# Optimization experiments

Hardware: AMD Instinct MI355X
Metric: run time of the kernel (lower is better)

## Reference

```python
import jax, jax.numpy as jnp
import numpy as np

N = 50000      # nodes
E = 800000     # edges
IN = 128       # in_channels
HID = 128      # hidden_channels
OUT = 2        # out_channels (edge classes)
HEADS = 8      # EGConv default num_heads
BASES = 4      # EGConv default num_bases
FH = HID // HEADS  # per-head feature dim = 16


def _egconv(x, Wb, Wc, bc, b, row, col, norm, n):
    """One EGConv layer (aggregators=['symnorm']), self-loops already in row/col/norm.
    Wb: [in, BASES*FH] basis projection (no bias).
    Wc: [in, HEADS*BASES], bc: combination weights linear.
    b : [HID] output bias.
    """
    bases = x @ Wb                                            # [n, BASES*FH]
    msg = bases[row] * norm[:, None]                          # gather + symnorm scale
    agg = jax.ops.segment_sum(msg, col, num_segments=n)       # scatter-add -> [n, BASES*FH]
    w = (x @ Wc + bc).reshape(n, HEADS, BASES)                # per-node combination weights
    out = jnp.einsum('nhb,nbf->nhf', w, agg.reshape(n, BASES, FH))
    return out.reshape(n, HEADS * FH) + b


def setup_inputs() -> dict:
    key = jax.random.key(0)
    ks = jax.random.split(key, 12)
    s = 0.05
    inp = {
        'x': jax.random.normal(ks[0], (N, IN), jnp.float32),
        'edge_index': jax.random.randint(ks[1], (2, E), 0, N, jnp.int64),
        # conv1
        'Wb1': jax.random.normal(ks[2], (IN, BASES * FH), jnp.float32) * s,
        'Wc1': jax.random.normal(ks[3], (IN, HEADS * BASES), jnp.float32) * s,
        'bc1': jnp.zeros((HEADS * BASES,), jnp.float32),
        'b1': jnp.zeros((HID,), jnp.float32),
        # conv2
        'Wb2': jax.random.normal(ks[4], (HID, BASES * FH), jnp.float32) * s,
        'Wc2': jax.random.normal(ks[5], (HID, HEADS * BASES), jnp.float32) * s,
        'bc2': jnp.zeros((HEADS * BASES,), jnp.float32),
        'b2': jnp.zeros((HID,), jnp.float32),
        # edge classifier
        'Wcls': jax.random.normal(ks[6], (2 * HID, OUT), jnp.float32) * s,
        'bcls': jnp.zeros((OUT,), jnp.float32),
    }
    return inp


def reference(x, edge_index, Wb1, Wc1, bc1, b1, Wb2, Wc2, bc2, b2, Wcls, bcls):
    n = x.shape[0]
    # add self loops (EGConv default add_self_loops=True) + gcn_norm symnorm weights
    sl = jnp.arange(n, dtype=edge_index.dtype)
    row = jnp.concatenate([edge_index[0], sl])
    col = jnp.concatenate([edge_index[1], sl])
    deg = jax.ops.segment_sum(jnp.ones(row.shape[0], x.dtype), col, num_segments=n)
    dis = jnp.where(deg > 0, deg, 1.0) ** -0.5
    dis = jnp.where(deg > 0, dis, 0.0)
    norm = dis[row] * dis[col]                                # symnorm edge weight

    h = jax.nn.relu(_egconv(x, Wb1, Wc1, bc1, b1, row, col, norm, n))
    h = _egconv(h, Wb2, Wc2, bc2, b2, row, col, norm, n)

    # edge classifier: gather endpoint embeddings of ORIGINAL edges, concat, linear
    e = jnp.concatenate([h[edge_index[0]], h[edge_index[1]]], axis=-1)  # [E, 2*HID]
    return e @ Wcls + bcls
```

## Files before the change

### kernel.cpp

```cpp
#include <hip/hip_runtime.h>
#include <hip/hip_fp16.h>

#define NN 50000
#define EE 800000
#define NB_E2 1563

__global__ void k_count(const int* __restrict__ ei, int* cnt) {
    int t = blockIdx.x * 256 + threadIdx.x;
    if (t < EE / 2) {
        int2 cc = *(const int2*)(ei + EE + 2 * t);
        atomicAdd(&cnt[cc.x], 1);
        atomicAdd(&cnt[cc.y], 1);
    }
}

__global__ void k_scan1(const int* __restrict__ cnt, int* sloc, int* bsum,
                        float* dis, int n) {
    __shared__ int s[256];
    int tid = threadIdx.x;
    int i = blockIdx.x * 256 + tid;
    int v = (i < n) ? cnt[i] : 0;
    if (i < n) dis[i] = rsqrtf((float)v + 1.0f);
    s[tid] = v;
    __syncthreads();
    for (int off = 1; off < 256; off <<= 1) {
        int t2 = 0;
        if (tid >= off) t2 = s[tid - off];
        __syncthreads();
        if (tid >= off) s[tid] += t2;
        __syncthreads();
    }
    if (i < n) sloc[i] = s[tid] - v;
    if (tid == 255) bsum[blockIdx.x] = s[255];
}

__global__ void k_scan23(const int* __restrict__ sloc, const int* __restrict__ bsum,
                         const int* __restrict__ cnt, int2* sd, int* cursor,
                         int n, int nb) {
    __shared__ int sb[256];
    int tid = threadIdx.x, b = blockIdx.x;
    int v = (tid < nb && tid < b) ? bsum[tid] : 0;
    sb[tid] = v;
    __syncthreads();
    for (int off = 128; off; off >>= 1) {
        if (tid < off) sb[tid] += sb[tid + off];
        __syncthreads();
    }
    int boff = sb[0];
    int i = b * 256 + tid;
    if (i < n) {
        int st = sloc[i] + boff;
        sd[i] = make_int2(st, cnt[i]);
        cursor[i] = st;
    }
}

__global__ void k_fill(const int* __restrict__ ei, int* cursor, int* __restrict__ csr) {
    int t = blockIdx.x * 256 + threadIdx.x;
    if (t < EE / 2) {
        int2 rr = *(const int2*)(ei + 2 * t);
        int2 cc = *(const int2*)(ei + EE + 2 * t);
        int p0 = atomicAdd(&cursor[cc.x], 1);
        csr[p0] = rr.x;
        int p1 = atomicAdd(&cursor[cc.y], 1);
        csr[p1] = rr.y;
    }
}

__global__ __launch_bounds__(256) void k_gemm(
    const float* __restrict__ x, const float* __restrict__ Wb,
    const float* __restrict__ Wc, const float* __restrict__ bc,
    const float* __restrict__ dis,
    __half* __restrict__ bsh, float* __restrict__ wcomb, int n)
{
    __shared__ float xt[32 * 257];
    int tid = threadIdx.x;
    int grp = blockIdx.y;
    int row0 = blockIdx.x * 256;
    int row = row0 + tid;
    bool valid = row < n;

    const float* W = (grp < 2) ? (Wb + grp * 32) : Wc;
    const int ldw = (grp < 2) ? 64 : 32;

    float acc[32];
#pragma unroll
    for (int c = 0; c < 32; c++) acc[c] = 0.f;

    for (int s = 0; s < 4; s++) {
        int base_k = s * 32;
        float4 v[8];
#pragma unroll
        for (int i = 0; i < 8; i++) {
            int idx = i * 256 + tid;
            int r = idx >> 3;
            int k4 = idx & 7;
            int gr = row0 + r;
            v[i] = (gr < n) ? *(const float4*)(x + (size_t)gr * 128 + base_k + k4 * 4)
                            : make_float4(0.f, 0.f, 0.f, 0.f);
        }
        __syncthreads();
#pragma unroll
        for (int i = 0; i < 8; i++) {
            int idx = i * 256 + tid;
            int r = idx >> 3;
            int k4 = idx & 7;
            xt[(k4 * 4 + 0) * 257 + r] = v[i].x;
            xt[(k4 * 4 + 1) * 257 + r] = v[i].y;
            xt[(k4 * 4 + 2) * 257 + r] = v[i].z;
            xt[(k4 * 4 + 3) * 257 + r] = v[i].w;
        }
        __syncthreads();

        const float* Ws = W + base_k * ldw;
#pragma unroll 8
        for (int k = 0; k < 32; k++) {
            float xs = xt[k * 257 + tid];
            const float* wk = Ws + k * ldw;
#pragma unroll
            for (int c = 0; c < 32; c++) acc[c] = fmaf(xs, wk[c], acc[c]);
        }
    }

    if (!valid) return;
    if (grp < 2) {
        float d = dis[row];
        __half2 hh[16];
#pragma unroll
        for (int c = 0; c < 16; c++)
            hh[c] = __floats2half2_rn(acc[2 * c] * d, acc[2 * c + 1] * d);
        uint4* bo = (uint4*)(bsh + (size_t)row * 64 + grp * 32);
        const uint4* src = (const uint4*)hh;
#pragma unroll
        for (int c = 0; c < 4; c++) bo[c] = src[c];
    } else {
        float4* wo = (float4*)(wcomb + (size_t)row * 32);
#pragma unroll
        for (int c = 0; c < 8; c++)
            wo[c] = make_float4(acc[4*c] + bc[4*c], acc[4*c+1] + bc[4*c+1],
                                acc[4*c+2] + bc[4*c+2], acc[4*c+3] + bc[4*c+3]);
    }
}

template<int LAYER2>
__global__ __launch_bounds__(256) void k_agg(
    const int* __restrict__ csr, const int2* __restrict__ sd,
    const __half* __restrict__ bsh, const float* __restrict__ dis,
    const float* __restrict__ wcomb, const float* __restrict__ bias,
    float* __restrict__ h,
    const float* __restrict__ Wcls, const float* __restrict__ bcls,
    float* __restrict__ p, int n)
{
    int wid = (blockIdx.x * 256 + threadIdx.x) >> 6;
    int lane = threadIdx.x & 63;
    if (wid >= n) return;
    int2 s2 = sd[wid];
    int start = s2.x, deg = s2.y;
    int g = lane >> 4, q = lane & 15;

    const uint2* bsp = (const uint2*)bsh;
    float4 acc4 = make_float4(0.f, 0.f, 0.f, 0.f);
    if (g == 0) {
        uint2 v = bsp[(size_t)wid * 16 + q];
        float2 lo = __half22float2(*(const __half2*)&v.x);
        float2 hi = __half22float2(*(const __half2*)&v.y);
        acc4 = make_float4(lo.x, lo.y, hi.x, hi.y);
    }

    int j = 0;
    int ia = 0, ib = 0;
    if (8 <= deg) { ia = csr[start + g]; ib = csr[start + 4 + g]; }
    while (j + 8 <= deg) {
        int jn = j + 8;
        int na = 0, nb = 0;
        if (jn + 8 <= deg) { na = csr[start + jn + g]; nb = csr[start + jn + 4 + g]; }
        uint2 v0 = bsp[(size_t)ia * 16 + q];
        uint2 v1 = bsp[(size_t)ib * 16 + q];
        float2 l0 = __half22float2(*(const __half2*)&v0.x);
        float2 h0 = __half22float2(*(const __half2*)&v0.y);
        float2 l1 = __half22float2(*(const __half2*)&v1.x);
        float2 h1 = __half22float2(*(const __half2*)&v1.y);
        acc4.x += l0.x + l1.x;
        acc4.y += l0.y + l1.y;
        acc4.z += h0.x + h1.x;
        acc4.w += h0.y + h1.y;
        ia = na; ib = nb; j = jn;
    }
    int last = start + deg - 1;
    for (; j < deg; j += 4) {
        int idx = start + j + g;
        int r = csr[min(idx, last)];
        uint2 v = bsp[(size_t)r * 16 + q];
        float2 lo = __half22float2(*(const __half2*)&v.x);
        float2 hi = __half22float2(*(const __half2*)&v.y);
        float m = (j + g < deg) ? 1.f : 0.f;
        acc4.x = fmaf(lo.x, m, acc4.x);
        acc4.y = fmaf(lo.y, m, acc4.y);
        acc4.z = fmaf(hi.x, m, acc4.z);
        acc4.w = fmaf(hi.y, m, acc4.w);
    }

    acc4.x += __shfl_xor(acc4.x, 16, 64);
    acc4.y += __shfl_xor(acc4.y, 16, 64);
    acc4.z += __shfl_xor(acc4.z, 16, 64);
    acc4.w += __shfl_xor(acc4.w, 16, 64);
    acc4.x += __shfl_xor(acc4.x, 32, 64);
    acc4.y += __shfl_xor(acc4.y, 32, 64);
    acc4.z += __shfl_xor(acc4.z, 32, 64);
    acc4.w += __shfl_xor(acc4.w, 32, 64);

    float d = dis[wid];
    acc4.x *= d; acc4.y *= d; acc4.z *= d; acc4.w *= d;

    int src = lane >> 2;
    float t0 = __shfl(acc4.x, src, 64);
    float t1 = __shfl(acc4.y, src, 64);
    float t2 = __shfl(acc4.z, src, 64);
    float t3 = __shfl(acc4.w, src, 64);
    int c = lane & 3;
    float acc = (c == 0) ? t0 : (c == 1) ? t1 : (c == 2) ? t2 : t3;

    int fh = lane & 15;
    float a0 = __shfl(acc, fh, 64);
    float a1 = __shfl(acc, 16 + fh, 64);
    float a2 = __shfl(acc, 32 + fh, 64);
    float a3 = __shfl(acc, 48 + fh, 64);
    const float* wn = wcomb + (size_t)wid * 32;
    int hd = lane >> 4;
    float s1 = bias[lane];
    float s2v = bias[64 + lane];
    s1 = fmaf(wn[hd * 4 + 0], a0, s1);
    s1 = fmaf(wn[hd * 4 + 1], a1, s1);
    s1 = fmaf(wn[hd * 4 + 2], a2, s1);
    s1 = fmaf(wn[hd * 4 + 3], a3, s1);
    s2v = fmaf(wn[(4 + hd) * 4 + 0], a0, s2v);
    s2v = fmaf(wn[(4 + hd) * 4 + 1], a1, s2v);
    s2v = fmaf(wn[(4 + hd) * 4 + 2], a2, s2v);
    s2v = fmaf(wn[(4 + hd) * 4 + 3], a3, s2v);

    if (!LAYER2) {
        s1 = fmaxf(s1, 0.f);
        s2v = fmaxf(s2v, 0.f);
        h[(size_t)wid * 128 + lane] = s1;
        h[(size_t)wid * 128 + 64 + lane] = s2v;
    } else {
        float r0 = s1 * Wcls[lane * 2 + 0] + s2v * Wcls[(64 + lane) * 2 + 0];
        float r1 = s1 * Wcls[lane * 2 + 1] + s2v * Wcls[(64 + lane) * 2 + 1];
        float r2 = s1 * Wcls[(128 + lane) * 2 + 0] + s2v * Wcls[(192 + lane) * 2 + 0];
        float r3 = s1 * Wcls[(128 + lane) * 2 + 1] + s2v * Wcls[(192 + lane) * 2 + 1];
#pragma unroll
        for (int off = 32; off; off >>= 1) {
            r0 += __shfl_xor(r0, off, 64);
            r1 += __shfl_xor(r1, off, 64);
            r2 += __shfl_xor(r2, off, 64);
            r3 += __shfl_xor(r3, off, 64);
        }
        if (lane == 0) {
            p[wid * 4 + 0] = r0 + bcls[0];
            p[wid * 4 + 1] = r1 + bcls[1];
            p[wid * 4 + 2] = r2;
            p[wid * 4 + 3] = r3;
        }
    }
}

__global__ void k_edge(const int* __restrict__ ei, const float* __restrict__ p,
                       float* __restrict__ out)
{
    int t = blockIdx.x * blockDim.x + threadIdx.x;
    if (t >= EE / 2) return;
    int2 rr = *(const int2*)(ei + 2 * t);
    int2 cc = *(const int2*)(ei + EE + 2 * t);
    float2 pt0 = *(const float2*)(p + rr.x * 4);
    float2 pt1 = *(const float2*)(p + rr.y * 4);
    float2 pb0 = *(const float2*)(p + cc.x * 4 + 2);
    float2 pb1 = *(const float2*)(p + cc.y * 4 + 2);
    float4 o;
    o.x = pt0.x + pb0.x;
    o.y = pt0.y + pb0.y;
    o.z = pt1.x + pb1.x;
    o.w = pt1.y + pb1.y;
    *(float4*)(out + (size_t)t * 4) = o;
}

extern "C" void kernel_launch(void* const* d_in, const int* in_sizes, int n_in,
                              void* d_out, int out_size, void* d_ws, size_t ws_size,
                              hipStream_t stream) {
    const float* x    = (const float*)d_in[0];
    const int*   ei   = (const int*)d_in[1];
    const float* Wb1  = (const float*)d_in[2];
    const float* Wc1  = (const float*)d_in[3];
    const float* bc1  = (const float*)d_in[4];
    const float* b1   = (const float*)d_in[5];
    const float* Wb2  = (const float*)d_in[6];
    const float* Wc2  = (const float*)d_in[7];
    const float* bc2  = (const float*)d_in[8];
    const float* b2   = (const float*)d_in[9];
    const float* Wcls = (const float*)d_in[10];
    const float* bcls = (const float*)d_in[11];
    float* out = (float*)d_out;

    char* ws = (char*)d_ws;
    size_t off = 0;
    auto alloc = [&](size_t bytes) {
        void* pp = ws + off;
        off += (bytes + 15) & ~(size_t)15;
        return pp;
    };

    float*  dis    = (float*)alloc(50048 * 4);
    __half* bsh    = (__half*)alloc((size_t)NN * 64 * 2);
    float*  wcomb  = (float*)alloc((size_t)NN * 32 * 4);
    float*  h      = (float*)alloc((size_t)NN * 128 * 4);
    float*  p      = (float*)alloc((size_t)NN * 4 * 4);
    int*    cnt    = (int*)alloc(50048 * 4);
    int*    sloc   = (int*)alloc(50048 * 4);
    int*    cursor = (int*)alloc(50048 * 4);
    int*    bsum   = (int*)alloc(256 * 4);
    int2*   sd     = (int2*)alloc((size_t)50048 * 8);
    int*    csr    = (int*)alloc((size_t)EE * 4);

    const int B = 256;
    int gN   = (NN + B - 1) / B;
    int gN64 = (NN * 64) / B;
    dim3 gG(gN, 3);

    hipMemsetAsync(cnt, 0, NN * sizeof(int), stream);
    k_count<<<NB_E2, B, 0, stream>>>(ei, cnt);
    k_scan1<<<gN, B, 0, stream>>>(cnt, sloc, bsum, dis, NN);
    k_scan23<<<gN, B, 0, stream>>>(sloc, bsum, cnt, sd, cursor, NN, gN);
    k_fill<<<NB_E2, B, 0, stream>>>(ei, cursor, csr);

    k_gemm<<<gG, B, 0, stream>>>(x, Wb1, Wc1, bc1, dis, bsh, wcomb, NN);
    k_agg<0><<<gN64, B, 0, stream>>>(csr, sd, bsh, dis, wcomb, b1, h,
                                     Wcls, bcls, p, NN);

    k_gemm<<<gG, B, 0, stream>>>(h, Wb2, Wc2, bc2, dis, bsh, wcomb, NN);
    k_agg<1><<<gN64, B, 0, stream>>>(csr, sd, bsh, dis, wcomb, b2, h,
                                     Wcls, bcls, p, NN);

    k_edge<<<NB_E2, B, 0, stream>>>(ei, p, out);
}
```

Measured before the change: 308.5 us.

## Build CSR from atomic ranks with destination-windowed scatter instead of fill atomics

k_count now records the rank returned by each atomicAdd, so k_fill can place every edge at starts[col]+rank without a second round of atomics on a cursor array. k_fill also splits the launch into 8 destination-node windows, and each window's blocks write only edges whose column falls in that window. The aim is to drop the contended fill atomics and to keep the scattered writes to csr and reads of starts within smaller address ranges for better cache locality. In exchange, the edge index and rank arrays are read 8 times, and a new E-sized rank buffer has to be written and read.

```diff
diff --git a/kernel.cpp b/kernel.cpp
--- a/kernel.cpp
+++ b/kernel.cpp
@@ -4,13 +4,17 @@
 #define NN 50000
 #define EE 800000
 #define NB_E2 1563
-
-__global__ void k_count(const int* __restrict__ ei, int* cnt) {
+#define WIN 6250
+#define EPB 1024
+#define NCHUNK 782
+
+__global__ void k_count(const int* __restrict__ ei, int* cnt, int* __restrict__ rank) {
     int t = blockIdx.x * 256 + threadIdx.x;
     if (t < EE / 2) {
         int2 cc = *(const int2*)(ei + EE + 2 * t);
-        atomicAdd(&cnt[cc.x], 1);
-        atomicAdd(&cnt[cc.y], 1);
+        int r0 = atomicAdd(&cnt[cc.x], 1);
+        int r1 = atomicAdd(&cnt[cc.y], 1);
+        *(int2*)(rank + 2 * t) = make_int2(r0, r1);
     }
 }
 
@@ -35,7 +39,7 @@
 }
 
 __global__ void k_scan23(const int* __restrict__ sloc, const int* __restrict__ bsum,
-                         const int* __restrict__ cnt, int2* sd, int* cursor,
+                         const int* __restrict__ cnt, int2* sd, int* starts,
                          int n, int nb) {
     __shared__ int sb[256];
     int tid = threadIdx.x, b = blockIdx.x;
@@ -51,19 +55,34 @@
     if (i < n) {
         int st = sloc[i] + boff;
         sd[i] = make_int2(st, cnt[i]);
-        cursor[i] = st;
-    }
-}
-
-__global__ void k_fill(const int* __restrict__ ei, int* cursor, int* __restrict__ csr) {
-    int t = blockIdx.x * 256 + threadIdx.x;
-    if (t < EE / 2) {
-        int2 rr = *(const int2*)(ei + 2 * t);
-        int2 cc = *(const int2*)(ei + EE + 2 * t);
-        int p0 = atomicAdd(&cursor[cc.x], 1);
-        csr[p0] = rr.x;
-        int p1 = atomicAdd(&cursor[cc.y], 1);
-        csr[p1] = rr.y;
+        starts[i] = st;
+    }
+}
+
+__global__ __launch_bounds__(256) void k_fill(
+    const int* __restrict__ ei, const int* __restrict__ rank,
+    const int* __restrict__ starts, int* __restrict__ csr)
+{
+    int w = blockIdx.x & 7;
+    int chunk = blockIdx.x >> 3;
+    int base = chunk * EPB + threadIdx.x * 4;
+    int lo = w * WIN, hi = lo + WIN;
+    if (base + 3 < EE) {
+        int4 rr = *(const int4*)(ei + base);
+        int4 cc = *(const int4*)(ei + EE + base);
+        int4 rk = *(const int4*)(rank + base);
+        if (cc.x >= lo && cc.x < hi) csr[starts[cc.x] + rk.x] = rr.x;
+        if (cc.y >= lo && cc.y < hi) csr[starts[cc.y] + rk.y] = rr.y;
+        if (cc.z >= lo && cc.z < hi) csr[starts[cc.z] + rk.z] = rr.z;
+        if (cc.w >= lo && cc.w < hi) csr[starts[cc.w] + rk.w] = rr.w;
+    } else {
+        for (int e = 0; e < 4; e++) {
+            int t = base + e;
+            if (t < EE) {
+                int c = ei[EE + t];
+                if (c >= lo && c < hi) csr[starts[c] + rank[t]] = ei[t];
+            }
+        }
     }
 }
 
@@ -315,10 +334,11 @@
     float*  p      = (float*)alloc((size_t)NN * 4 * 4);
     int*    cnt    = (int*)alloc(50048 * 4);
     int*    sloc   = (int*)alloc(50048 * 4);
-    int*    cursor = (int*)alloc(50048 * 4);
+    int*    starts = (int*)alloc(50048 * 4);
     int*    bsum   = (int*)alloc(256 * 4);
     int2*   sd     = (int2*)alloc((size_t)50048 * 8);
     int*    csr    = (int*)alloc((size_t)EE * 4);
+    int*    rank   = (int*)alloc((size_t)EE * 4);
 
     const int B = 256;
     int gN   = (NN + B - 1) / B;
@@ -326,10 +346,10 @@
     dim3 gG(gN, 3);
 
     hipMemsetAsync(cnt, 0, NN * sizeof(int), stream);
-    k_count<<<NB_E2, B, 0, stream>>>(ei, cnt);
+    k_count<<<NB_E2, B, 0, stream>>>(ei, cnt, rank);
     k_scan1<<<gN, B, 0, stream>>>(cnt, sloc, bsum, dis, NN);
-    k_scan23<<<gN, B, 0, stream>>>(sloc, bsum, cnt, sd, cursor, NN, gN);
-    k_fill<<<NB_E2, B, 0, stream>>>(ei, cursor, csr);
+    k_scan23<<<gN, B, 0, stream>>>(sloc, bsum, cnt, sd, starts, NN, gN);
+    k_fill<<<NCHUNK * 8, B, 0, stream>>>(ei, rank, starts, csr);
 
     k_gemm<<<gG, B, 0, stream>>>(x, Wb1, Wc1, bc1, dis, bsh, wcomb, NN);
     k_agg<0><<<gN64, B, 0, stream>>>(csr, sd, bsh, dis, wcomb, b1, h,
```

Result: faster. 277.7 us (-10.0%).
